# Kernel tuning notes

Measured on AMD Instinct MI355X. Metric: run time of the kernel, lower is better.

The kernel has to match this reference:

```python
import jax, jax.numpy as jnp
import numpy as np


def _conv(x, k):
    # x: (B,H,W,Cin), k: (kh,kw,Cin,Cout), SAME padding, stride 1
    return jax.lax.conv_general_dilated(
        x, k, window_strides=(1, 1), padding='SAME',
        dimension_numbers=('NHWC', 'HWIO', 'NHWC'))


def _hard_sigmoid(x):
    # Keras ConvLSTM2D default recurrent_activation='hard_sigmoid'
    return jnp.clip(0.2 * x + 0.5, 0.0, 1.0)


def _convlstm_layer(x_seq, k, rk, b):
    # x_seq: (B,T,H,W,Cin); gates packed i,f,c,o along channel axis (Keras order)
    B, T, H, W, _ = x_seq.shape
    F = rk.shape[2]
    h0 = jnp.zeros((B, H, W, F), x_seq.dtype)
    c0 = jnp.zeros((B, H, W, F), x_seq.dtype)

    def step(carry, xt):
        h, c = carry
        z = _conv(xt, k) + _conv(h, rk) + b
        i, f, g, o = jnp.split(z, 4, axis=-1)
        c_new = _hard_sigmoid(f) * c + _hard_sigmoid(i) * jnp.tanh(g)
        h_new = _hard_sigmoid(o) * jnp.tanh(c_new)
        return (h_new, c_new), h_new

    (h, c), ys = jax.lax.scan(step, (h0, c0), jnp.moveaxis(x_seq, 1, 0))
    return jnp.moveaxis(ys, 0, 1), h, c  # outputs (B,T,H,W,F), final h, c


def setup_inputs() -> dict:
    key = jax.random.key(0)
    ks = jax.random.split(key, 6)
    s = 0.05
    return {
        'x': jax.random.normal(ks[0], (8, 10, 64, 64, 1), jnp.float32),
        'k0': jax.random.normal(ks[1], (3, 3, 1, 256), jnp.float32) * s,
        'rk0': jax.random.normal(ks[2], (3, 3, 64, 256), jnp.float32) * s,
        'b0': jnp.zeros((256,), jnp.float32),
        'k1': jax.random.normal(ks[3], (3, 3, 64, 256), jnp.float32) * s,
        'rk1': jax.random.normal(ks[4], (3, 3, 64, 256), jnp.float32) * s,
        'b1': jnp.zeros((256,), jnp.float32),
    }


def reference(x, k0, rk0, b0, k1, rk1, b1):
    # layer 0
    seq0, h0, c0 = _convlstm_layer(x, k0, rk0, b0)
    # layer 1 consumes layer-0 sequence
    _, h1, c1 = _convlstm_layer(seq0, k1, rk1, b1)
    # states list [[h0,c0],[h1,c1]] -> stacked (layers=2, 2, B, H, W, F)
    return jnp.stack([jnp.stack([h0, c0]), jnp.stack([h1, c1])])
```

## Files before the change

kernel.cpp:

```cpp
#include <hip/hip_runtime.h>
#include <hip/hip_bf16.h>

typedef unsigned short u16;
typedef __attribute__((ext_vector_type(8))) short short8;
typedef __attribute__((ext_vector_type(4))) float f32x4;

#define T_STEPS 10
#define NB 8
#define HH 64
#define WW 64
#define FF 64
#define NGATE 256
#define HP 66
#define PIX (NB*HH*WW)

__device__ __forceinline__ u16 f2bf(float f) {
    unsigned u = __float_as_uint(f);
    u += 0x7FFF + ((u >> 16) & 1);
    return (u16)(u >> 16);
}
__device__ __forceinline__ float hsig(float x) {
    return fminf(fmaxf(0.2f * x + 0.5f, 0.0f), 1.0f);
}
__device__ __forceinline__ float ftanh(float x) {
    float e = __expf(2.0f * x);
    return 1.0f - 2.0f / (e + 1.0f);
}
__device__ __forceinline__ void gll16(const void* g, void* l) {
    __builtin_amdgcn_global_load_lds(
        (const __attribute__((address_space(1))) unsigned*)g,
        (__attribute__((address_space(3))) unsigned*)l, 16, 0, 0);
}

__global__ void wtrans_kernel(const float* __restrict__ W0,
                              const float* __restrict__ W1,
                              u16* __restrict__ BS, int K) {
    int total = (K >> 6) << 14;
    for (int o = blockIdx.x * blockDim.x + threadIdx.x; o < total;
         o += gridDim.x * blockDim.x) {
        int e = o & 7, lane = (o >> 3) & 63, g = (o >> 9) & 3;
        int ks = (o >> 11) & 1, fq = (o >> 12) & 3, kc = o >> 14;
        int quad = lane >> 4, l15 = lane & 15;
        int n = g * 64 + fq * 16 + l15;
        int k = kc * 64 + ks * 32 + quad * 8 + e;
        float v = (k < 576) ? W0[k * NGATE + n] : W1[(k - 576) * NGATE + n];
        BS[o] = f2bf(v);
    }
}

__device__ __forceinline__ void stageA(const u16* __restrict__ h0_prev,
                                       const u16* __restrict__ h1_prev,
                                       int kcs, int b, int y, int tid,
                                       u16* __restrict__ lbase) {
    int tau = (kcs < 9) ? kcs : kcs - 9;
    const u16* src = (kcs < 9) ? h0_prev : h1_prev;
    int dy = tau / 3 - 1, dx = tau % 3 - 1;
    const u16* rbase = src + (((size_t)(b * HP + y + dy + 1)) * HP + dx + 1) * FF;
    int q0 = tid, q1 = 256 + tid;
    int p0 = q0 >> 3, cb0 = (q0 & 7) ^ (p0 & 7);
    int p1 = q1 >> 3, cb1 = (q1 & 7) ^ (p1 & 7);
    gll16(rbase + (size_t)p0 * FF + cb0 * 8, lbase + (size_t)q0 * 8);
    gll16(rbase + (size_t)p1 * FF + cb1 * 8, lbase + (size_t)q1 * 8);
}

__global__ __launch_bounds__(256, 4)
void fused_step_kernel(const u16* __restrict__ h0_prev, u16* __restrict__ h0_new,
                       const u16* __restrict__ h1_prev, u16* __restrict__ h1_new,
                       const u16* __restrict__ B0S, const u16* __restrict__ B1S,
                       const float* __restrict__ x, const float* __restrict__ k0w,
                       const float* __restrict__ b0, const float* __restrict__ b1,
                       float* __restrict__ c0, float* __restrict__ c1,
                       float* __restrict__ oh0, float* __restrict__ oc0,
                       float* __restrict__ oh1, float* __restrict__ oc1,
                       int u) {
    int blk = blockIdx.x;
    int b = blk & 7;
    int k = blk >> 3;
    int role = (k >> 5) & 1;
    int y = (k & 31) | ((k >> 6) << 5);
    int pxb = b * 64 + y;
    if (role == 0 && u >= T_STEPS) return;
    if (role == 1 && u == 0) return;

    __shared__ __align__(16) u16 sA3[3][4096];
    __shared__ float xs[3][WW + 2];

    int tid = threadIdx.x;
    int lane = tid & 63, fq = tid >> 6;
    int quad = lane >> 4, l15 = lane & 15;

    const u16* BS = role ? B1S : B0S;
    int nch = role ? 18 : 9;

    if (role == 0 && tid < 3 * (WW + 2)) {
        int dyi = tid / (WW + 2), xx = tid - dyi * (WW + 2);
        int yy = y + dyi - 1, col = xx - 1;
        float v = 0.0f;
        if (yy >= 0 && yy < HH && col >= 0 && col < WW)
            v = x[(((size_t)b * T_STEPS + u) * HH + yy) * WW + col];
        xs[dyi][xx] = v;
    }

    f32x4 acc[4][4];
#pragma unroll
    for (int mt = 0; mt < 4; ++mt)
#pragma unroll
        for (int g = 0; g < 4; ++g)
            acc[mt][g] = (f32x4){0.f, 0.f, 0.f, 0.f};

    stageA(h0_prev, h1_prev, 0, b, y, tid, &sA3[0][0]);
    asm volatile("s_waitcnt vmcnt(0) lgkmcnt(0)\n\ts_barrier" ::: "memory");
    if (nch > 1)
        stageA(h0_prev, h1_prev, 1, b, y, tid, &sA3[1][0]);

    int sx = l15 & 7;
    int cur = 0;
    for (int kc = 0; kc < nch; ++kc) {
#pragma unroll
        for (int ks = 0; ks < 2; ++ks) {
            short8 bF[4];
            const u16* bp = BS + (((size_t)kc << 14) | (fq << 12) | (ks << 11))
                          + lane * 8;
#pragma unroll
            for (int g = 0; g < 4; ++g)
                bF[g] = *(const short8*)(bp + ((size_t)g << 9));
            short8 aF[4];
#pragma unroll
            for (int mt = 0; mt < 4; ++mt) {
                int px = mt * 16 + l15;
                int chunk = px * 8 + ((ks * 4 + quad) ^ sx);
                aF[mt] = *(const short8*)&sA3[cur][(size_t)chunk * 8];
            }
            __builtin_amdgcn_s_setprio(1);
#pragma unroll
            for (int mt = 0; mt < 4; ++mt)
#pragma unroll
                for (int g = 0; g < 4; ++g)
                    acc[mt][g] = __builtin_amdgcn_mfma_f32_16x16x32_bf16(
                        aF[mt], bF[g], acc[mt][g], 0, 0, 0);
            __builtin_amdgcn_s_setprio(0);
        }
        {
            int ksrc = (kc + 2 < nch) ? kc + 2 : kc;
            int bdst = (cur + 2 >= 3) ? cur - 1 : cur + 2;
            stageA(h0_prev, h1_prev, ksrc, b, y, tid, &sA3[bdst][0]);
        }
        asm volatile("s_waitcnt vmcnt(2) lgkmcnt(0)\n\ts_barrier" ::: "memory");
        cur = (cur == 2) ? 0 : cur + 1;
    }

    const float* bias = role ? b1 : b0;
    float* cbuf = role ? c1 : c0;
    u16* hout = role ? h1_new : h0_new;
    int wo = role ? (u == T_STEPS) : (u == T_STEPS - 1);
    float* outh = role ? oh1 : oh0;
    float* outc = role ? oc1 : oc0;

    int f = fq * 16 + l15;
    float bi = bias[f], bff = bias[64 + f], bg = bias[128 + f], bo = bias[192 + f];
    float wk[4][9];
    if (role == 0) {
#pragma unroll
        for (int g = 0; g < 4; ++g)
#pragma unroll
            for (int tau = 0; tau < 9; ++tau)
                wk[g][tau] = k0w[tau * NGATE + g * 64 + f];
    }
#pragma unroll
    for (int mt = 0; mt < 4; ++mt) {
#pragma unroll
        for (int r = 0; r < 4; ++r) {
            int xcol = mt * 16 + quad * 4 + r;
            size_t p = (size_t)pxb * 64 + xcol;
            float zi = acc[mt][0][r] + bi;
            float zf = acc[mt][1][r] + bff;
            float zg = acc[mt][2][r] + bg;
            float zo = acc[mt][3][r] + bo;
            if (role == 0) {
#pragma unroll
                for (int tau = 0; tau < 9; ++tau) {
                    float xv = xs[tau / 3][xcol + tau % 3];
                    zi += xv * wk[0][tau];
                    zf += xv * wk[1][tau];
                    zg += xv * wk[2][tau];
                    zo += xv * wk[3][tau];
                }
            }
            float cold = cbuf[p * FF + f];
            float cn = hsig(zf) * cold + hsig(zi) * ftanh(zg);
            float hn = hsig(zo) * ftanh(cn);
            cbuf[p * FF + f] = cn;
            hout[(((size_t)(b * HP + y + 1)) * HP + (xcol + 1)) * FF + f] = f2bf(hn);
            if (wo) { outh[p * FF + f] = hn; outc[p * FF + f] = cn; }
        }
    }
}

extern "C" void kernel_launch(void* const* d_in, const int* in_sizes, int n_in,
                              void* d_out, int out_size, void* d_ws, size_t ws_size,
                              hipStream_t stream) {
    const float* x   = (const float*)d_in[0];
    const float* k0  = (const float*)d_in[1];
    const float* rk0 = (const float*)d_in[2];
    const float* b0  = (const float*)d_in[3];
    const float* k1  = (const float*)d_in[4];
    const float* rk1 = (const float*)d_in[5];
    const float* b1  = (const float*)d_in[6];
    float* out = (float*)d_out;

    char* ws = (char*)d_ws;
    const size_t HPAD_BYTES = (size_t)NB * HP * HP * FF * 2;
    const size_t C_BYTES    = (size_t)PIX * FF * 4;

    u16* h0p[2]; u16* h1p[2];
    h0p[0] = (u16*)(ws);
    h0p[1] = (u16*)(ws + HPAD_BYTES);
    h1p[0] = (u16*)(ws + 2 * HPAD_BYTES);
    h1p[1] = (u16*)(ws + 3 * HPAD_BYTES);
    float* c0 = (float*)(ws + 4 * HPAD_BYTES);
    float* c1 = (float*)(ws + 4 * HPAD_BYTES + C_BYTES);
    u16* B0S  = (u16*)(ws + 4 * HPAD_BYTES + 2 * C_BYTES);
    u16* B1S  = (u16*)(ws + 4 * HPAD_BYTES + 2 * C_BYTES + (size_t)9 * 16384 * 2);

    hipMemsetAsync(ws, 0, 4 * HPAD_BYTES + 2 * C_BYTES, stream);

    wtrans_kernel<<<512, 256, 0, stream>>>(rk0, rk0, B0S, 576);
    wtrans_kernel<<<512, 256, 0, stream>>>(k1, rk1, B1S, 1152);

    float* oh0 = out;
    float* oc0 = out + (size_t)PIX * FF;
    float* oh1 = out + 2 * (size_t)PIX * FF;
    float* oc1 = out + 3 * (size_t)PIX * FF;

    for (int u = 0; u <= T_STEPS; ++u) {
        const u16* h0_prev = h0p[(u + 1) & 1];
        u16*       h0_new  = h0p[u & 1];
        const u16* h1_prev = h1p[u & 1];
        u16*       h1_new  = h1p[(u + 1) & 1];
        fused_step_kernel<<<1024, 256, 0, stream>>>(
            h0_prev, h0_new, h1_prev, h1_new, B0S, B1S,
            x, k0, b0, b1, c0, c1, oh0, oc0, oh1, oc1, u);
    }
}
```

Measured before the change: 492.2 us.

## Load A operands directly from global memory instead of LDS triple-buffer

Drops the LDS triple-buffered staging of the h-state tiles (global_load_lds with swizzle and per-chunk barriers). Each wave now reads its A fragments straight from global memory, relying on L1/L2 to serve the 4x redundant reads across the four wave groups. This removes the barriers and the LDS traffic, at the cost of more global/cache requests and less latency hiding. The launch-bounds occupancy hint is also lowered from 4 to 3.

```diff
diff --git a/kernel.cpp b/kernel.cpp
--- a/kernel.cpp
+++ b/kernel.cpp
@@ -25,11 +25,6 @@
 __device__ __forceinline__ float ftanh(float x) {
     float e = __expf(2.0f * x);
     return 1.0f - 2.0f / (e + 1.0f);
-}
-__device__ __forceinline__ void gll16(const void* g, void* l) {
-    __builtin_amdgcn_global_load_lds(
-        (const __attribute__((address_space(1))) unsigned*)g,
-        (__attribute__((address_space(3))) unsigned*)l, 16, 0, 0);
 }
 
 __global__ void wtrans_kernel(const float* __restrict__ W0,
@@ -48,22 +43,7 @@
     }
 }
 
-__device__ __forceinline__ void stageA(const u16* __restrict__ h0_prev,
-                                       const u16* __restrict__ h1_prev,
-                                       int kcs, int b, int y, int tid,
-                                       u16* __restrict__ lbase) {
-    int tau = (kcs < 9) ? kcs : kcs - 9;
-    const u16* src = (kcs < 9) ? h0_prev : h1_prev;
-    int dy = tau / 3 - 1, dx = tau % 3 - 1;
-    const u16* rbase = src + (((size_t)(b * HP + y + dy + 1)) * HP + dx + 1) * FF;
-    int q0 = tid, q1 = 256 + tid;
-    int p0 = q0 >> 3, cb0 = (q0 & 7) ^ (p0 & 7);
-    int p1 = q1 >> 3, cb1 = (q1 & 7) ^ (p1 & 7);
-    gll16(rbase + (size_t)p0 * FF + cb0 * 8, lbase + (size_t)q0 * 8);
-    gll16(rbase + (size_t)p1 * FF + cb1 * 8, lbase + (size_t)q1 * 8);
-}
-
-__global__ __launch_bounds__(256, 4)
+__global__ __launch_bounds__(256, 3)
 void fused_step_kernel(const u16* __restrict__ h0_prev, u16* __restrict__ h0_new,
                        const u16* __restrict__ h1_prev, u16* __restrict__ h1_new,
                        const u16* __restrict__ B0S, const u16* __restrict__ B1S,
@@ -82,7 +62,6 @@
     if (role == 0 && u >= T_STEPS) return;
     if (role == 1 && u == 0) return;
 
-    __shared__ __align__(16) u16 sA3[3][4096];
     __shared__ float xs[3][WW + 2];
 
     int tid = threadIdx.x;
@@ -108,46 +87,34 @@
         for (int g = 0; g < 4; ++g)
             acc[mt][g] = (f32x4){0.f, 0.f, 0.f, 0.f};
 
-    stageA(h0_prev, h1_prev, 0, b, y, tid, &sA3[0][0]);
-    asm volatile("s_waitcnt vmcnt(0) lgkmcnt(0)\n\ts_barrier" ::: "memory");
-    if (nch > 1)
-        stageA(h0_prev, h1_prev, 1, b, y, tid, &sA3[1][0]);
-
-    int sx = l15 & 7;
-    int cur = 0;
+    int aoff = l15 * FF + quad * 8;
+    const u16* bbase = BS + (fq << 12) + lane * 8;
+
     for (int kc = 0; kc < nch; ++kc) {
+        int tau = (kc < 9) ? kc : kc - 9;
+        const u16* src = (kc < 9) ? h0_prev : h1_prev;
+        const u16* ab = src
+            + (((size_t)(b * HP + y + tau / 3)) * HP + tau % 3) * FF + aoff;
+        const u16* bp = bbase + ((size_t)kc << 14);
 #pragma unroll
         for (int ks = 0; ks < 2; ++ks) {
-            short8 bF[4];
-            const u16* bp = BS + (((size_t)kc << 14) | (fq << 12) | (ks << 11))
-                          + lane * 8;
+            short8 bF[4], aF[4];
 #pragma unroll
             for (int g = 0; g < 4; ++g)
-                bF[g] = *(const short8*)(bp + ((size_t)g << 9));
-            short8 aF[4];
-#pragma unroll
-            for (int mt = 0; mt < 4; ++mt) {
-                int px = mt * 16 + l15;
-                int chunk = px * 8 + ((ks * 4 + quad) ^ sx);
-                aF[mt] = *(const short8*)&sA3[cur][(size_t)chunk * 8];
-            }
-            __builtin_amdgcn_s_setprio(1);
+                bF[g] = *(const short8*)(bp + (ks << 11) + (g << 9));
+#pragma unroll
+            for (int mt = 0; mt < 4; ++mt)
+                aF[mt] = *(const short8*)(ab + mt * 16 * FF + ks * 32);
 #pragma unroll
             for (int mt = 0; mt < 4; ++mt)
 #pragma unroll
                 for (int g = 0; g < 4; ++g)
                     acc[mt][g] = __builtin_amdgcn_mfma_f32_16x16x32_bf16(
                         aF[mt], bF[g], acc[mt][g], 0, 0, 0);
-            __builtin_amdgcn_s_setprio(0);
         }
-        {
-            int ksrc = (kc + 2 < nch) ? kc + 2 : kc;
-            int bdst = (cur + 2 >= 3) ? cur - 1 : cur + 2;
-            stageA(h0_prev, h1_prev, ksrc, b, y, tid, &sA3[bdst][0]);
-        }
-        asm volatile("s_waitcnt vmcnt(2) lgkmcnt(0)\n\ts_barrier" ::: "memory");
-        cur = (cur == 2) ? 0 : cur + 1;
-    }
+    }
+
+    if (role == 0) __syncthreads();
 
     const float* bias = role ? b1 : b0;
     float* cbuf = role ? c1 : c0;
```

After: 804.7 us. 1.64x slower.
